# Optimization experiments

Measured on AMD Instinct MI355X. Metric: run time of the kernel, lower is better.

Reference implementation:

```python
import jax, jax.numpy as jnp
import numpy as np
from jax import lax

FACTOR = 2
FIR = (1.0, 3.0, 3.0, 1.0)


def _fir_kernel():
    k1 = jnp.array(FIR, dtype=jnp.float32)
    k = jnp.outer(k1, k1)
    k = k / jnp.sum(k)
    return k * (FACTOR ** 2)  # gain=1, factor=2 -> x4


def _upfirdn2d(x, kernel, up, down, pad):
    # x: [N, C, H, W]; kernel: [kh, kw]; faithful to upfirdn2d_native:
    # upsample by zero-insertion (lhs_dilation), pad, convolve with flipped
    # kernel (F.conv2d is correlation of flipped kernel == true convolution),
    # then downsample by striding. lax.conv_general_dilated is correlation,
    # so pass the flipped kernel.
    C = x.shape[1]
    kflip = kernel[::-1, ::-1]
    w = jnp.tile(kflip[None, None], (C, 1, 1, 1))  # depthwise [C,1,kh,kw]
    return lax.conv_general_dilated(
        x, w,
        window_strides=(down, down),
        padding=[(pad[0], pad[1]), (pad[0], pad[1])],
        lhs_dilation=(up, up),
        feature_group_count=C,
        dimension_numbers=("NCHW", "OIHW", "NCHW"),
    )


def setup_inputs() -> dict:
    key = jax.random.key(0)
    k1, k2, k3 = jax.random.split(key, 3)
    N, C, H, W = 8, 256, 64, 64
    outC = 256
    hidden_states = jax.random.normal(k1, (N, C, H, W), dtype=jnp.float32)
    weight = jax.random.normal(k2, (outC, C, 3, 3), dtype=jnp.float32) * 0.05
    bias = jax.random.normal(k3, (outC,), dtype=jnp.float32)
    return {"hidden_states": hidden_states, "weight": weight, "bias": bias}


def reference(hidden_states, weight, bias):
    # FirUpsample2D.forward with use_conv=True, fir_kernel=(1,3,3,1), factor=2.
    k = _fir_kernel()  # [4, 4]
    convH, convW = weight.shape[2], weight.shape[3]
    pad_value = k.shape[0] - FACTOR - (convW - 1)  # = 0 here

    # The torch code flips+channel-swaps the weight then calls conv_transpose2d
    # (which itself flips and channel-swaps); the two cancel, so the net op is
    # plain cross-correlation of the ORIGINAL weight over the factor-dilated
    # input with (kH-1) padding on each side (output_padding == 0).
    x = lax.conv_general_dilated(
        hidden_states, weight,
        window_strides=(1, 1),
        padding=[(convH - 1, convH - 1), (convW - 1, convW - 1)],
        lhs_dilation=(FACTOR, FACTOR),
        dimension_numbers=("NCHW", "OIHW", "NCHW"),
    )  # [N, outC, (H-1)*2+3, (W-1)*2+3]

    out = _upfirdn2d(
        x, k, up=1, down=1,
        pad=((pad_value + 1) // 2 + FACTOR - 1, pad_value // 2 + 1),
    )  # [N, outC, 2H, 2W]

    return out + bias[None, :, None, None]
```

## Files before the change

### kernel.cpp

```cpp
#include <hip/hip_runtime.h>
#include <cstdint>
#include <cstddef>

typedef _Float16 f16;
typedef _Float16 f16x8 __attribute__((ext_vector_type(8)));
typedef float f32x4 __attribute__((ext_vector_type(4)));

#define AS1 __attribute__((address_space(1)))
#define AS3 __attribute__((address_space(3)))

__device__ __forceinline__ void gl_lds16(const void* g, void* l) {
  __builtin_amdgcn_global_load_lds((AS1 void*)g, (AS3 void*)l, 16u, 0, 0u);
}

__constant__ float c_tab[2][3][3] = {
  {{0.75f, 0.25f, 0.00f}, {0.25f, 0.75f, 0.75f}, {0.00f, 0.00f, 0.25f}},
  {{0.25f, 0.00f, 0.00f}, {0.75f, 0.75f, 0.25f}, {0.00f, 0.25f, 0.75f}}
};

__global__ __launch_bounds__(256) void prep_k(const float* __restrict__ W,
                                              const float* __restrict__ In,
                                              f16* __restrict__ Et,
                                              f16* __restrict__ Ah) {
  const int b = blockIdx.x;
  const int tid = threadIdx.x;
  if (b < 256) {
    const int oc = b;
    const int ic = tid;
    const int c = ic >> 5, icl = ic & 31;
    float w[9];
    const float* wp = W + ((size_t)oc * 256 + ic) * 9;
#pragma unroll
    for (int t = 0; t < 9; ++t) w[t] = wp[t];
#pragma unroll
    for (int py = 0; py < 2; ++py)
#pragma unroll
      for (int px = 0; px < 2; ++px) {
        const int jj = oc * 4 + py * 2 + px;
#pragma unroll
        for (int ay = 0; ay < 3; ++ay)
#pragma unroll
          for (int ax = 0; ax < 3; ++ax) {
            float s = 0.f;
#pragma unroll
            for (int iy = 0; iy < 3; ++iy)
#pragma unroll
              for (int ix = 0; ix < 3; ++ix)
                s += w[iy * 3 + ix] * c_tab[py][ay][iy] * c_tab[px][ax][ix];
            Et[((size_t)(((c * 3 + ay) * 3 + ax) * 1024 + jj)) * 32 + icl] = (f16)s;
          }
      }
  } else {
    const int bid2 = b - 256;
    const int icc = bid2 & 7;
    const int v = bid2 >> 3;
    const int n = v / 66;
    const int yp = v - n * 66;
    const int ic0 = icc * 32;
    const int icl = tid & 31, x8 = tid >> 5;
    f16* rowbase = Ah + ((size_t)(n * 66 + yp) * 66) * 256 + ic0;
    if (yp == 0 || yp == 65) {
#pragma unroll
      for (int i = 0; i < 9; ++i) {
        const int xp = i * 8 + x8;
        if (xp < 66) rowbase[(size_t)xp * 256 + icl] = (f16)0.f;
      }
    } else {
      const int y = yp - 1;
      __shared__ float tile[32][65];
      const int xl = tid & 63, icl4 = tid >> 6;
      const float* src = In + (((size_t)(n * 256 + ic0)) * 64 + y) * 64;
#pragma unroll
      for (int i = 0; i < 8; ++i) {
        const int icl_ = i * 4 + icl4;
        tile[icl_][xl] = src[(size_t)icl_ * 4096 + xl];
      }
      __syncthreads();
      f16* dst = rowbase + 256;
#pragma unroll
      for (int i = 0; i < 8; ++i) {
        const int x = i * 8 + x8;
        dst[(size_t)x * 256 + icl] = (f16)tile[icl][x];
      }
      if (x8 == 0) {
        rowbase[icl] = (f16)0.f;
        rowbase[(size_t)65 * 256 + icl] = (f16)0.f;
      }
    }
  }
}

__global__ __launch_bounds__(256) void gemm_k(const f16* __restrict__ Ah,
                                              const f16* __restrict__ Et,
                                              const float* __restrict__ bias,
                                              float* __restrict__ out) {
  __shared__ __align__(16) f16 lA[4224];
  __shared__ __align__(16) f16 lB[12288];
  const int tid = threadIdx.x;
  const int wave = tid >> 6;
  const int lane = tid & 63;
  const int bid = blockIdx.x;
  const int nt = bid & 7;
  const int mt = bid >> 3;
  const int m0 = mt * 128;
  const int jj0 = nt * 128;
  const int n = m0 >> 12;
  const int y0 = (m0 >> 6) & 63;

  int goA[2];
#pragma unroll
  for (int i = 0; i < 2; ++i) {
    const int s = wave * 2 + i;
    const int u = s * 16 + (lane >> 2);
    const int row = (u >= 66) ? 1 : 0;
    const int x = u - 66 * row;
    goA[i] = ((row * 66 + x) * 256 + (lane & 3) * 8) * 2;
  }
  const int goAt = ((66 + 62 + (lane >> 2)) * 256 + (lane & 3) * 8) * 2;
  int goB[6];
#pragma unroll
  for (int j = 0; j < 6; ++j) {
    const int t = wave + 4 * j;
    const int ax = t >> 3, sub = t & 7;
    goB[j] = (ax * 32768 + (sub * 16 + (lane >> 2)) * 32 + (lane & 3) * 8) * 2;
  }
  char* const lAb = (char*)lA;
  char* const lBb = (char*)lB;
  char* const dA0 = lAb + (wave * 2 + 0) * 1024;
  char* const dA1 = lAb + (wave * 2 + 1) * 1024;
  char* const dAt = lAb + 8192;

  const int wm = wave >> 1, wn = wave & 1;
  const int lr = lane & 15;
  const int base_a = wm * 4224 + lr * 64 + (lane >> 4) * 16;
  const int base_b = (wn * 64 + lr) * 64 + (lane >> 4) * 16;

  const char* const aN = (const char*)Ah + (size_t)(n * 66 + y0) * 33792;
  const char* const bE = (const char*)Et + (size_t)jj0 * 64;

  const f32x4 vzero = {0.f, 0.f, 0.f, 0.f};
  f32x4 acc[4][4];
#pragma unroll
  for (int i = 0; i < 4; ++i)
#pragma unroll
    for (int j = 0; j < 4; ++j) acc[i][j] = vzero;

#pragma unroll 1
  for (int c = 0; c < 8; ++c) {
#pragma unroll 1
    for (int ay = 0; ay < 3; ++ay) {
      const char* aP = aN + ay * 33792 + c * 64;
      const char* bP = bE + (size_t)(c * 3 + ay) * 196608;

      __syncthreads();
      gl_lds16(aP + goA[0], dA0);
      gl_lds16(aP + goA[1], dA1);
      if (wave == 3 && lane < 16) gl_lds16(aP + goAt, dAt);
#pragma unroll
      for (int j = 0; j < 6; ++j) gl_lds16(bP + goB[j], lBb + (wave + 4 * j) * 1024);
      __syncthreads();

#pragma unroll
      for (int ax = 0; ax < 3; ++ax) {
        f16x8 af[4], bf[4];
#pragma unroll
        for (int mi = 0; mi < 4; ++mi)
          af[mi] = *(const f16x8*)(lAb + base_a + (mi * 16 + ax) * 64);
#pragma unroll
        for (int ni = 0; ni < 4; ++ni)
          bf[ni] = *(const f16x8*)(lBb + base_b + ax * 8192 + ni * 1024);
#pragma unroll
        for (int mi = 0; mi < 4; ++mi)
#pragma unroll
          for (int ni = 0; ni < 4; ++ni)
            acc[mi][ni] =
                __builtin_amdgcn_mfma_f32_16x16x32_f16(af[mi], bf[ni], acc[mi][ni], 0, 0, 0);
      }
    }
  }

  const int yw = y0 + wm;
#pragma unroll
  for (int ni = 0; ni < 4; ++ni) {
    const int jj = jj0 + wn * 64 + ni * 16 + lr;
    const int oc = jj >> 2;
    const int py = (jj >> 1) & 1, px = jj & 1;
    const float bv = bias[oc];
    const int oy = 2 * yw + py;
    float* orow = out + ((size_t)(n * 256 + oc) * 128 + oy) * 128;
#pragma unroll
    for (int mi = 0; mi < 4; ++mi) {
      const int xb = mi * 16 + ((lane >> 4) << 2);
#pragma unroll
      for (int v = 0; v < 4; ++v) {
        orow[2 * (xb + v) + px] = acc[mi][ni][v] + bv;
      }
    }
  }
}

__global__ __launch_bounds__(256) void fallback_k(const float* __restrict__ In,
                                                  const float* __restrict__ W,
                                                  const float* __restrict__ bias,
                                                  float* __restrict__ out) {
  const size_t idx = (size_t)blockIdx.x * 256 + threadIdx.x;
  const int ox = (int)(idx & 127), oy = (int)((idx >> 7) & 127);
  const int oc = (int)((idx >> 14) & 255);
  const int n = (int)(idx >> 22);
  const int px = ox & 1, py = oy & 1;
  const int x = ox >> 1, y = oy >> 1;
  float cy[3][3], cx[3][3];
#pragma unroll
  for (int a = 0; a < 3; ++a)
#pragma unroll
    for (int i = 0; i < 3; ++i) {
      cy[a][i] = c_tab[py][a][i];
      cx[a][i] = c_tab[px][a][i];
    }
  float acc = 0.f;
  const float* wbase = W + (size_t)oc * 2304;
  for (int ic = 0; ic < 256; ++ic) {
    const float* ib = In + (((size_t)(n * 256 + ic)) * 64 + y) * 64 + x;
    float pin[3][3];
#pragma unroll
    for (int ay = 0; ay < 3; ++ay) {
      const int yy = y + ay - 1;
#pragma unroll
      for (int ax = 0; ax < 3; ++ax) {
        const int xx = x + ax - 1;
        pin[ay][ax] = (yy >= 0 && yy < 64 && xx >= 0 && xx < 64)
                          ? ib[(ay - 1) * 64 + (ax - 1)] : 0.f;
      }
    }
    const float* w = wbase + ic * 9;
    float U[3][3];
#pragma unroll
    for (int ay = 0; ay < 3; ++ay)
#pragma unroll
      for (int ix = 0; ix < 3; ++ix)
        U[ay][ix] = cx[0][ix] * pin[ay][0] + cx[1][ix] * pin[ay][1] + cx[2][ix] * pin[ay][2];
#pragma unroll
    for (int iy = 0; iy < 3; ++iy)
#pragma unroll
      for (int ix = 0; ix < 3; ++ix) {
        const float V = cy[0][iy] * U[0][ix] + cy[1][iy] * U[1][ix] + cy[2][iy] * U[2][ix];
        acc += w[iy * 3 + ix] * V;
      }
  }
  out[idx] = acc + bias[oc];
}

extern "C" void kernel_launch(void* const* d_in, const int* in_sizes, int n_in,
                              void* d_out, int out_size, void* d_ws, size_t ws_size,
                              hipStream_t stream) {
  const float* In = (const float*)d_in[0];
  const float* W = (const float*)d_in[1];
  const float* bias = (const float*)d_in[2];
  float* out = (float*)d_out;

  const size_t E_BYTES = (size_t)1024 * 2304 * 2;
  const size_t A_BYTES = (size_t)8 * 66 * 66 * 256 * 2;

  if (ws_size >= E_BYTES + A_BYTES) {
    f16* Et = (f16*)d_ws;
    f16* Ah = (f16*)((char*)d_ws + E_BYTES);
    prep_k<<<256 + 4224, 256, 0, stream>>>(W, In, Et, Ah);
    gemm_k<<<2048, 256, 0, stream>>>(Ah, Et, bias, out);
  } else {
    fallback_k<<<131072, 256, 0, stream>>>(In, W, bias, out);
  }
}
```

Before: 334.8 us.

## Double-buffer LDS tiles in GEMM and XOR-swizzle LDS layout

Converts the GEMM main loop to double-buffered LDS, so the global-to-LDS loads for the next (c, ay) step are issued while MFMAs run on the current buffer, leaving one barrier per iteration instead of two. It also applies an XOR swizzle to the 16-byte chunk index on both the global source offsets and the LDS read addresses to reduce bank conflicts. Register pressure rises because all three ax fragment sets are preloaded, and LDS usage doubles, which could lower occupancy.

```diff
diff --git a/kernel.cpp b/kernel.cpp
--- a/kernel.cpp
+++ b/kernel.cpp
@@ -94,8 +94,8 @@
                                               const f16* __restrict__ Et,
                                               const float* __restrict__ bias,
                                               float* __restrict__ out) {
-  __shared__ __align__(16) f16 lA[4224];
-  __shared__ __align__(16) f16 lB[12288];
+  __shared__ __align__(256) f16 lA[2][4224];
+  __shared__ __align__(256) f16 lB[2][12288];
   const int tid = threadIdx.x;
   const int wave = tid >> 6;
   const int lane = tid & 63;
@@ -107,6 +107,7 @@
   const int n = m0 >> 12;
   const int y0 = (m0 >> 6) & 63;
 
+  const int hig = (lane & 3) ^ ((lane >> 3) & 3);
   int goA[2];
 #pragma unroll
   for (int i = 0; i < 2; ++i) {
@@ -114,26 +115,38 @@
     const int u = s * 16 + (lane >> 2);
     const int row = (u >= 66) ? 1 : 0;
     const int x = u - 66 * row;
-    goA[i] = ((row * 66 + x) * 256 + (lane & 3) * 8) * 2;
-  }
-  const int goAt = ((66 + 62 + (lane >> 2)) * 256 + (lane & 3) * 8) * 2;
+    goA[i] = ((row * 66 + x) * 256 + hig * 8) * 2;
+  }
+  const int goAt = ((66 + 62 + (lane >> 2)) * 256 + hig * 8) * 2;
   int goB[6];
 #pragma unroll
   for (int j = 0; j < 6; ++j) {
     const int t = wave + 4 * j;
     const int ax = t >> 3, sub = t & 7;
-    goB[j] = (ax * 32768 + (sub * 16 + (lane >> 2)) * 32 + (lane & 3) * 8) * 2;
+    goB[j] = (ax * 32768 + (sub * 16 + (lane >> 2)) * 32 + hig * 8) * 2;
   }
   char* const lAb = (char*)lA;
   char* const lBb = (char*)lB;
-  char* const dA0 = lAb + (wave * 2 + 0) * 1024;
-  char* const dA1 = lAb + (wave * 2 + 1) * 1024;
-  char* const dAt = lAb + 8192;
 
   const int wm = wave >> 1, wn = wave & 1;
   const int lr = lane & 15;
-  const int base_a = wm * 4224 + lr * 64 + (lane >> 4) * 16;
-  const int base_b = (wn * 64 + lr) * 64 + (lane >> 4) * 16;
+  const int hi16 = (lane >> 4) * 16;
+  int rdA[4][3];
+#pragma unroll
+  for (int mi = 0; mi < 4; ++mi)
+#pragma unroll
+    for (int ax = 0; ax < 3; ++ax) {
+      const int o = wm * 4224 + (lr + mi * 16 + ax) * 64 + hi16;
+      rdA[mi][ax] = o ^ (((o >> 7) & 3) << 4);
+    }
+  int rdB[4][3];
+#pragma unroll
+  for (int ni = 0; ni < 4; ++ni)
+#pragma unroll
+    for (int ax = 0; ax < 3; ++ax) {
+      const int o = (wn * 64 + lr) * 64 + hi16 + ax * 8192 + ni * 1024;
+      rdB[ni][ax] = o ^ (((o >> 7) & 3) << 4);
+    }
 
   const char* const aN = (const char*)Ah + (size_t)(n * 66 + y0) * 33792;
   const char* const bE = (const char*)Et + (size_t)jj0 * 64;
@@ -145,38 +158,57 @@
 #pragma unroll
     for (int j = 0; j < 4; ++j) acc[i][j] = vzero;
 
+  {
+    gl_lds16(aN + goA[0], lAb + (wave * 2 + 0) * 1024);
+    gl_lds16(aN + goA[1], lAb + (wave * 2 + 1) * 1024);
+    if (wave == 3 && lane < 16) gl_lds16(aN + goAt, lAb + 8192);
+#pragma unroll
+    for (int j = 0; j < 6; ++j) gl_lds16(bE + goB[j], lBb + (wave + 4 * j) * 1024);
+  }
+  __syncthreads();
+
+  const char* aPn = aN + 33792;
+  const char* bPn = bE + 196608;
+  int ayn = 1;
+
 #pragma unroll 1
-  for (int c = 0; c < 8; ++c) {
-#pragma unroll 1
-    for (int ay = 0; ay < 3; ++ay) {
-      const char* aP = aN + ay * 33792 + c * 64;
-      const char* bP = bE + (size_t)(c * 3 + ay) * 196608;
-
-      __syncthreads();
-      gl_lds16(aP + goA[0], dA0);
-      gl_lds16(aP + goA[1], dA1);
-      if (wave == 3 && lane < 16) gl_lds16(aP + goAt, dAt);
-#pragma unroll
-      for (int j = 0; j < 6; ++j) gl_lds16(bP + goB[j], lBb + (wave + 4 * j) * 1024);
-      __syncthreads();
-
-#pragma unroll
-      for (int ax = 0; ax < 3; ++ax) {
-        f16x8 af[4], bf[4];
-#pragma unroll
-        for (int mi = 0; mi < 4; ++mi)
-          af[mi] = *(const f16x8*)(lAb + base_a + (mi * 16 + ax) * 64);
+  for (int t = 0; t < 24; ++t) {
+    const int p = t & 1;
+    const char* sA = lAb + p * 8448;
+    const char* sB = lBb + p * 24576;
+
+    f16x8 af[3][4], bf[3][4];
+#pragma unroll
+    for (int ax = 0; ax < 3; ++ax) {
+#pragma unroll
+      for (int mi = 0; mi < 4; ++mi) af[ax][mi] = *(const f16x8*)(sA + rdA[mi][ax]);
+#pragma unroll
+      for (int ni = 0; ni < 4; ++ni) bf[ax][ni] = *(const f16x8*)(sB + rdB[ni][ax]);
+    }
+
+    if (t < 23) {
+      char* dA = lAb + (p ^ 1) * 8448;
+      char* dB = lBb + (p ^ 1) * 24576;
+      gl_lds16(aPn + goA[0], dA + (wave * 2 + 0) * 1024);
+      gl_lds16(aPn + goA[1], dA + (wave * 2 + 1) * 1024);
+      if (wave == 3 && lane < 16) gl_lds16(aPn + goAt, dA + 8192);
+#pragma unroll
+      for (int j = 0; j < 6; ++j) gl_lds16(bPn + goB[j], dB + (wave + 4 * j) * 1024);
+      bPn += 196608;
+      if (ayn == 2) { aPn -= 67520; ayn = 0; }
+      else          { aPn += 33792; ++ayn; }
+    }
+
+#pragma unroll
+    for (int ax = 0; ax < 3; ++ax)
+#pragma unroll
+      for (int mi = 0; mi < 4; ++mi)
 #pragma unroll
         for (int ni = 0; ni < 4; ++ni)
-          bf[ni] = *(const f16x8*)(lBb + base_b + ax * 8192 + ni * 1024);
-#pragma unroll
-        for (int mi = 0; mi < 4; ++mi)
-#pragma unroll
-          for (int ni = 0; ni < 4; ++ni)
-            acc[mi][ni] =
-                __builtin_amdgcn_mfma_f32_16x16x32_f16(af[mi], bf[ni], acc[mi][ni], 0, 0, 0);
-      }
-    }
+          acc[mi][ni] = __builtin_amdgcn_mfma_f32_16x16x32_f16(af[ax][mi], bf[ax][ni],
+                                                               acc[mi][ni], 0, 0, 0);
+
+    __syncthreads();
   }
 
   const int yw = y0 + wm;
```

Result: no change. 329.4 us (-1.6%).
